# Kernel tuning notes

Measured on AMD Instinct MI355X. Metric: run time of the kernel, lower is better.

## Reference

```python
import jax, jax.numpy as jnp
import numpy as np

N = 50000
E = 800000
F_IN = 128
HID = 64
HEADS = 4
NEG_SLOPE = 0.2  # PyG GATConv default negative_slope


def segment_softmax(e, dst, num_segments):
    # numerically stable softmax over edges grouped by destination node
    m = jax.ops.segment_max(e, dst, num_segments=num_segments)
    ex = jnp.exp(e - m[dst])
    s = jax.ops.segment_sum(ex, dst, num_segments=num_segments)
    return ex / (s[dst] + 1e-16)


def gat_conv(x, src, dst, W, a_src, a_dst, bias, heads, out_ch, concat):
    n = x.shape[0]
    h = (x @ W).reshape(n, heads, out_ch)          # [N,H,C]
    alpha_s = (h * a_src).sum(-1)                  # [N,H]
    alpha_d = (h * a_dst).sum(-1)                  # [N,H]
    e = jax.nn.leaky_relu(alpha_s[src] + alpha_d[dst], NEG_SLOPE)  # [E,H]
    alpha = segment_softmax(e, dst, n)             # [E,H]
    out = jax.ops.segment_sum(h[src] * alpha[:, :, None], dst, num_segments=n)  # [N,H,C]
    out = out.reshape(n, heads * out_ch) if concat else out.mean(axis=1)
    return out + bias


def setup_inputs() -> dict:
    key = jax.random.key(0)
    ks = jax.random.split(key, 16)

    def lin(k, i, o):
        return (jax.random.normal(k, (i, o), jnp.float32) / np.float32(np.sqrt(i)))

    def att(k, h, c):
        return jax.random.normal(k, (h, c), jnp.float32) * np.float32(0.1)

    x = jax.random.normal(ks[0], (N, F_IN), jnp.float32)
    edge_index = jax.random.randint(ks[1], (2, E), 0, N, dtype=jnp.int32)
    return {
        "x": x,
        "W_emb": lin(ks[2], F_IN, HID), "b_emb": jnp.zeros(HID, jnp.float32),
        "W0": lin(ks[3], HID, HEADS * HID), "as0": att(ks[4], HEADS, HID), "ad0": att(ks[5], HEADS, HID), "b0": jnp.zeros(HEADS * HID, jnp.float32),
        "W1": lin(ks[6], HEADS * HID, HEADS * HID), "as1": att(ks[7], HEADS, HID), "ad1": att(ks[8], HEADS, HID), "b1": jnp.zeros(HEADS * HID, jnp.float32),
        "W2": lin(ks[9], HEADS * HID, HID), "as2": att(ks[10], 1, HID), "ad2": att(ks[11], 1, HID), "b2": jnp.zeros(HID, jnp.float32),
        "Wo1": lin(ks[12], HID, HID // 2), "bo1": jnp.zeros(HID // 2, jnp.float32),
        "Wo2": lin(ks[13], HID // 2, 1), "bo2": jnp.zeros(1, jnp.float32),
        "edge_index": edge_index,
    }


def reference(x, W_emb, b_emb, W0, as0, ad0, b0, W1, as1, ad1, b1, W2, as2, ad2, b2, Wo1, bo1, Wo2, bo2, edge_index):
    n = x.shape[0]
    loop = jnp.arange(n, dtype=edge_index.dtype)  # PyG GATConv adds self-loops
    src = jnp.concatenate([edge_index[0], loop])
    dst = jnp.concatenate([edge_index[1], loop])
    h = jax.nn.relu(x @ W_emb + b_emb)
    h = jax.nn.relu(gat_conv(h, src, dst, W0, as0, ad0, b0, HEADS, HID, True))   # dropout=identity (eval)
    h = jax.nn.relu(gat_conv(h, src, dst, W1, as1, ad1, b1, HEADS, HID, True))
    h = gat_conv(h, src, dst, W2, as2, ad2, b2, 1, HID, False)
    h = jax.nn.relu(h @ Wo1 + bo1)
    return h @ Wo2 + bo2  # [N,1]
```

## Files before the change

kernel.cpp:

```cpp
#include <hip/hip_runtime.h>

typedef _Float16 h8_t __attribute__((ext_vector_type(8)));
typedef _Float16 h4_t __attribute__((ext_vector_type(4)));
typedef float floatx4 __attribute__((ext_vector_type(4)));

__device__ __forceinline__ float leaky(float v) { return v >= 0.f ? v : 0.2f * v; }

__global__ void hist_kernel(const int* __restrict__ dst, int E, int* __restrict__ cnt) {
    int e = blockIdx.x * blockDim.x + threadIdx.x;
    if (e < E) atomicAdd(&cnt[dst[e]], 1);
}

__global__ __launch_bounds__(256) void blocksum_kernel(const int* __restrict__ cnt, int N,
                                                       int* __restrict__ bsum) {
    __shared__ int red[256];
    int tid = threadIdx.x;
    int idx = blockIdx.x * 256 + tid;
    red[tid] = idx < N ? cnt[idx] + 1 : 0;
    __syncthreads();
#pragma unroll
    for (int off = 128; off >= 1; off >>= 1) {
        if (tid < off) red[tid] += red[tid + off];
        __syncthreads();
    }
    if (tid == 0) bsum[blockIdx.x] = red[0];
}

__global__ __launch_bounds__(256) void scanbsum_kernel(int* __restrict__ bsum, int nb,
                                                       int* __restrict__ total) {
    __shared__ int part[256];
    int tid = threadIdx.x;
    int per = (nb + 255) / 256;
    int s0 = tid * per, s1 = min(s0 + per, nb);
    int s = 0;
    for (int i = s0; i < s1; i++) s += bsum[i];
    part[tid] = s;
    __syncthreads();
    for (int off = 1; off < 256; off <<= 1) {
        int v = (tid >= off) ? part[tid - off] : 0;
        __syncthreads();
        part[tid] += v;
        __syncthreads();
    }
    int base = (tid == 0) ? 0 : part[tid - 1];
    for (int i = s0; i < s1; i++) {
        int v = bsum[i];
        bsum[i] = base;
        base += v;
    }
    if (tid == 255) *total = part[255];
}

__global__ __launch_bounds__(256) void rowptr_kernel(const int* __restrict__ cnt,
                                                     const int* __restrict__ bsum, int N,
                                                     int* __restrict__ row_ptr,
                                                     int* __restrict__ cursor) {
    __shared__ int lds[256];
    int tid = threadIdx.x;
    int idx = blockIdx.x * 256 + tid;
    int v = idx < N ? cnt[idx] + 1 : 0;
    lds[tid] = v;
    __syncthreads();
    for (int off = 1; off < 256; off <<= 1) {
        int t = (tid >= off) ? lds[tid - off] : 0;
        __syncthreads();
        lds[tid] += t;
        __syncthreads();
    }
    if (idx < N) {
        int p = bsum[blockIdx.x] + lds[tid] - v;
        row_ptr[idx] = p;
        cursor[idx] = p;
    }
}

__global__ void scatter_kernel(const int* __restrict__ src, const int* __restrict__ dst,
                               int E, int N, int* __restrict__ cursor, int* __restrict__ csr_src) {
    int e = blockIdx.x * blockDim.x + threadIdx.x;
    if (e >= E + N) return;
    int s, d;
    if (e < E) { s = src[e]; d = dst[e]; }
    else       { s = e - E;  d = s; }
    int pos = atomicAdd(&cursor[d], 1);
    csr_src[pos] = s;
}

__global__ void prep_weights_all(const float* __restrict__ W_emb, const float* __restrict__ W0,
                                 const float* __restrict__ W1, const float* __restrict__ W2,
                                 _Float16* __restrict__ WeH, _Float16* __restrict__ WeL,
                                 _Float16* __restrict__ W0H, _Float16* __restrict__ W0L,
                                 _Float16* __restrict__ W1H, _Float16* __restrict__ W1L,
                                 _Float16* __restrict__ W2H, _Float16* __restrict__ W2L) {
    int which = blockIdx.y;
    const float* W;
    _Float16 *Wh, *Wl;
    int K, N;
    if (which == 0)      { W = W_emb; Wh = WeH; Wl = WeL; K = 128; N = 64; }
    else if (which == 1) { W = W0;    Wh = W0H; Wl = W0L; K = 64;  N = 256; }
    else if (which == 2) { W = W1;    Wh = W1H; Wl = W1L; K = 256; N = 256; }
    else                 { W = W2;    Wh = W2H; Wl = W2L; K = 256; N = 64; }
    int idx = blockIdx.x * blockDim.x + threadIdx.x;
    if (idx >= K * N) return;
    int k = idx / N, n = idx % N;
    float v = W[idx];
    _Float16 hi = (_Float16)v;
    _Float16 lo = (_Float16)(v - (float)hi);
    size_t o = ((size_t)(k >> 3) * N + n) * 8 + (k & 7);
    Wh[o] = hi; Wl[o] = lo;
}

__global__ void prep_act_kernel(const float* __restrict__ X,
                                _Float16* __restrict__ Ph, _Float16* __restrict__ Pl,
                                int M, int Mpad, int Kg, int K) {
    int idx = blockIdx.x * blockDim.x + threadIdx.x;
    if (idx >= Mpad * Kg) return;
    int row = idx / Kg, kg = idx - row * Kg;
    float vs[8] = {0.f, 0.f, 0.f, 0.f, 0.f, 0.f, 0.f, 0.f};
    if (row < M) {
        const float4* p = (const float4*)(X + (size_t)row * K + kg * 8);
        float4 a = p[0], b = p[1];
        vs[0] = a.x; vs[1] = a.y; vs[2] = a.z; vs[3] = a.w;
        vs[4] = b.x; vs[5] = b.y; vs[6] = b.z; vs[7] = b.w;
    }
    h8_t hh, hl;
#pragma unroll
    for (int j = 0; j < 8; j++) {
        _Float16 hi = (_Float16)vs[j];
        hh[j] = hi;
        hl[j] = (_Float16)(vs[j] - (float)hi);
    }
    size_t o = ((size_t)kg * Mpad + row) * 8;
    *reinterpret_cast<h8_t*>(Ph + o) = hh;
    *reinterpret_cast<h8_t*>(Pl + o) = hl;
}

__global__ __launch_bounds__(256) void gemm_emb_kernel(
        const _Float16* __restrict__ Ah, const _Float16* __restrict__ Al,
        const _Float16* __restrict__ Bh, const _Float16* __restrict__ Bl,
        const float* __restrict__ bias,
        _Float16* __restrict__ Ph, _Float16* __restrict__ Pl,
        int Mpad, int M, int K) {
    const int Nn = 64;
    __shared__ _Float16 Bs[2][4][64][8];
    __shared__ _Float16 stH[4][16][72];
    __shared__ _Float16 stL[4][16][72];
    int tid = threadIdx.x;
    int wv = tid >> 6, lane = tid & 63;
    int m16 = lane & 15, quad = lane >> 4;
    int row0 = blockIdx.x * 128 + wv * 32;

    floatx4 acc[2][4];
#pragma unroll
    for (int t = 0; t < 2; t++)
#pragma unroll
        for (int c = 0; c < 4; c++)
#pragma unroll
            for (int i = 0; i < 4; i++) acc[t][c][i] = 0.f;

    size_t aoff = ((size_t)quad * Mpad + row0 + m16) * 8;
    size_t kqbase = 0;
    const size_t aStep = (size_t)Mpad * 32;
    const size_t bStep = (size_t)Nn * 32;

    for (int kt = 0; kt < K; kt += 32) {
        h8_t ah0 = *reinterpret_cast<const h8_t*>(Ah + aoff);
        h8_t ah1 = *reinterpret_cast<const h8_t*>(Ah + aoff + 128);
        h8_t al0 = *reinterpret_cast<const h8_t*>(Al + aoff);
        h8_t al1 = *reinterpret_cast<const h8_t*>(Al + aoff + 128);
#pragma unroll
        for (int cc = 0; cc < 2; cc++) {
            int c = tid + cc * 256;
            int plane = c >> 8, rem = c & 255, q = rem >> 6, col = rem & 63;
            const _Float16* srcp = (plane ? Bl : Bh) + kqbase + ((size_t)q * Nn + col) * 8;
            *reinterpret_cast<h8_t*>(&Bs[plane][q][col][0]) = *reinterpret_cast<const h8_t*>(srcp);
        }
        __syncthreads();
#pragma unroll
        for (int c = 0; c < 4; c++) {
            h8_t bh = *reinterpret_cast<const h8_t*>(&Bs[0][quad][c * 16 + m16][0]);
            h8_t bl = *reinterpret_cast<const h8_t*>(&Bs[1][quad][c * 16 + m16][0]);
            acc[0][c] = __builtin_amdgcn_mfma_f32_16x16x32_f16(ah0, bh, acc[0][c], 0, 0, 0);
            acc[1][c] = __builtin_amdgcn_mfma_f32_16x16x32_f16(ah1, bh, acc[1][c], 0, 0, 0);
            acc[0][c] = __builtin_amdgcn_mfma_f32_16x16x32_f16(ah0, bl, acc[0][c], 0, 0, 0);
            acc[1][c] = __builtin_amdgcn_mfma_f32_16x16x32_f16(ah1, bl, acc[1][c], 0, 0, 0);
            acc[0][c] = __builtin_amdgcn_mfma_f32_16x16x32_f16(al0, bh, acc[0][c], 0, 0, 0);
            acc[1][c] = __builtin_amdgcn_mfma_f32_16x16x32_f16(al1, bh, acc[1][c], 0, 0, 0);
        }
        __syncthreads();
        aoff += aStep; kqbase += bStep;
    }

#pragma unroll
    for (int t = 0; t < 2; t++) {
#pragma unroll
        for (int c = 0; c < 4; c++) {
            float bv = bias[c * 16 + m16];
#pragma unroll
            for (int i = 0; i < 4; i++) {
                float v = fmaxf(acc[t][c][i] + bv, 0.f);
                _Float16 hi = (_Float16)v;
                stH[wv][quad * 4 + i][c * 16 + m16] = hi;
                stL[wv][quad * 4 + i][c * 16 + m16] = (_Float16)(v - (float)hi);
            }
        }
        __syncthreads();
        int rowChunk = row0 + t * 16;
#pragma unroll
        for (int it = 0; it < 2; it++) {
            int lid = it * 64 + lane;
            int kg = lid >> 4, rloc = lid & 15;
            h8_t vh = *reinterpret_cast<const h8_t*>(&stH[wv][rloc][kg * 8]);
            h8_t vl = *reinterpret_cast<const h8_t*>(&stL[wv][rloc][kg * 8]);
            size_t o = ((size_t)kg * Mpad + rowChunk + rloc) * 8;
            *reinterpret_cast<h8_t*>(Ph + o) = vh;
            *reinterpret_cast<h8_t*>(Pl + o) = vl;
        }
        __syncthreads();
    }
}

template <int TAG>
__global__ __launch_bounds__(256) void gemm_gat_kernel(
        const _Float16* __restrict__ Ah, const _Float16* __restrict__ Al,
        const _Float16* __restrict__ Bh, const _Float16* __restrict__ Bl,
        const float* __restrict__ a_src, const float* __restrict__ a_dst,
        _Float16* __restrict__ hOut, float* __restrict__ aS, float* __restrict__ aD,
        int Mpad, int M, int K) {
    const int Nn = 256;
    __shared__ _Float16 Bs[2][4][128][8];
    __shared__ _Float16 st[4][16][136];
    int tid = threadIdx.x;
    int wv = tid >> 6, lane = tid & 63;
    int m16 = lane & 15, quad = lane >> 4;
    int row0 = blockIdx.x * 128 + wv * 32;
    int colBase = blockIdx.y * 128;

    floatx4 acc[2][8];
#pragma unroll
    for (int t = 0; t < 2; t++)
#pragma unroll
        for (int c = 0; c < 8; c++)
#pragma unroll
            for (int i = 0; i < 4; i++) acc[t][c][i] = 0.f;

    size_t aoff = ((size_t)quad * Mpad + row0 + m16) * 8;
    size_t kqbase = (size_t)colBase * 8;
    const size_t aStep = (size_t)Mpad * 32;
    const size_t bStep = (size_t)Nn * 32;

    for (int kt = 0; kt < K; kt += 32) {
        h8_t ah0 = *reinterpret_cast<const h8_t*>(Ah + aoff);
        h8_t ah1 = *reinterpret_cast<const h8_t*>(Ah + aoff + 128);
        h8_t al0 = *reinterpret_cast<const h8_t*>(Al + aoff);
        h8_t al1 = *reinterpret_cast<const h8_t*>(Al + aoff + 128);
#pragma unroll
        for (int cc = 0; cc < 4; cc++) {
            int c = tid + cc * 256;
            int plane = c >> 9, rem = c & 511, q = rem >> 7, col = rem & 127;
            const _Float16* srcp = (plane ? Bl : Bh) + kqbase + ((size_t)q * Nn + col) * 8;
            *reinterpret_cast<h8_t*>(&Bs[plane][q][col][0]) = *reinterpret_cast<const h8_t*>(srcp);
        }
        __syncthreads();
#pragma unroll
        for (int c = 0; c < 8; c++) {
            h8_t bh = *reinterpret_cast<const h8_t*>(&Bs[0][quad][c * 16 + m16][0]);
            h8_t bl = *reinterpret_cast<const h8_t*>(&Bs[1][quad][c * 16 + m16][0]);
            acc[0][c] = __builtin_amdgcn_mfma_f32_16x16x32_f16(ah0, bh, acc[0][c], 0, 0, 0);
            acc[1][c] = __builtin_amdgcn_mfma_f32_16x16x32_f16(ah1, bh, acc[1][c], 0, 0, 0);
            acc[0][c] = __builtin_amdgcn_mfma_f32_16x16x32_f16(ah0, bl, acc[0][c], 0, 0, 0);
            acc[1][c] = __builtin_amdgcn_mfma_f32_16x16x32_f16(ah1, bl, acc[1][c], 0, 0, 0);
            acc[0][c] = __builtin_amdgcn_mfma_f32_16x16x32_f16(al0, bh, acc[0][c], 0, 0, 0);
            acc[1][c] = __builtin_amdgcn_mfma_f32_16x16x32_f16(al1, bh, acc[1][c], 0, 0, 0);
        }
        __syncthreads();
        aoff += aStep; kqbase += bStep;
    }

    float asv[8], adv[8];
#pragma unroll
    for (int c = 0; c < 8; c++) {
        asv[c] = a_src[colBase + c * 16 + m16];
        adv[c] = a_dst[colBase + c * 16 + m16];
    }
    int hb = colBase >> 6;
#pragma unroll
    for (int t = 0; t < 2; t++) {
#pragma unroll
        for (int i = 0; i < 4; i++) {
            int r = row0 + t * 16 + quad * 4 + i;
            float s0 = 0.f, d0 = 0.f, s1 = 0.f, d1 = 0.f;
#pragma unroll
            for (int c = 0; c < 8; c++) {
                float v = acc[t][c][i];
                if (c < 4) { s0 += v * asv[c]; d0 += v * adv[c]; }
                else       { s1 += v * asv[c]; d1 += v * adv[c]; }
            }
#pragma unroll
            for (int off = 1; off < 16; off <<= 1) {
                s0 += __shfl_xor(s0, off);
                d0 += __shfl_xor(d0, off);
                s1 += __shfl_xor(s1, off);
                d1 += __shfl_xor(d1, off);
            }
            if (m16 == 0 && r < M) {
                aS[r * 4 + hb] = s0;     aD[r * 4 + hb] = d0;
                aS[r * 4 + hb + 1] = s1; aD[r * 4 + hb + 1] = d1;
            }
        }
    }

#pragma unroll
    for (int t = 0; t < 2; t++) {
#pragma unroll
        for (int c = 0; c < 8; c++)
#pragma unroll
            for (int i = 0; i < 4; i++)
                st[wv][quad * 4 + i][c * 16 + m16] = (_Float16)acc[t][c][i];
        __syncthreads();
        int rowChunk = row0 + t * 16;
#pragma unroll
        for (int it = 0; it < 4; it++) {
            int lid = it * 64 + lane;
            int rloc = lid >> 4, u = lid & 15;
            h8_t v = *reinterpret_cast<const h8_t*>(&st[wv][rloc][u * 8]);
            *reinterpret_cast<h8_t*>(hOut + (size_t)(rowChunk + rloc) * 256 + colBase + u * 8) = v;
        }
        __syncthreads();
    }
}

__global__ __launch_bounds__(256) void gemm_l2_kernel(
        const _Float16* __restrict__ Ah, const _Float16* __restrict__ Al,
        const _Float16* __restrict__ Bh, const _Float16* __restrict__ Bl,
        const float* __restrict__ a_src, const float* __restrict__ a_dst,
        _Float16* __restrict__ hOut, float* __restrict__ aS, float* __restrict__ aD,
        int Mpad, int M, int K) {
    const int Nn = 64;
    __shared__ _Float16 Bs[2][4][64][8];
    __shared__ _Float16 st[4][16][72];
    int tid = threadIdx.x;
    int wv = tid >> 6, lane = tid & 63;
    int m16 = lane & 15, quad = lane >> 4;
    int row0 = blockIdx.x * 128 + wv * 32;

    floatx4 acc[2][4];
#pragma unroll
    for (int t = 0; t < 2; t++)
#pragma unroll
        for (int c = 0; c < 4; c++)
#pragma unroll
            for (int i = 0; i < 4; i++) acc[t][c][i] = 0.f;

    size_t aoff = ((size_t)quad * Mpad + row0 + m16) * 8;
    size_t kqbase = 0;
    const size_t aStep = (size_t)Mpad * 32;
    const size_t bStep = (size_t)Nn * 32;

    for (int kt = 0; kt < K; kt += 32) {
        h8_t ah0 = *reinterpret_cast<const h8_t*>(Ah + aoff);
        h8_t ah1 = *reinterpret_cast<const h8_t*>(Ah + aoff + 128);
        h8_t al0 = *reinterpret_cast<const h8_t*>(Al + aoff);
        h8_t al1 = *reinterpret_cast<const h8_t*>(Al + aoff + 128);
#pragma unroll
        for (int cc = 0; cc < 2; cc++) {
            int c = tid + cc * 256;
            int plane = c >> 8, rem = c & 255, q = rem >> 6, col = rem & 63;
            const _Float16* srcp = (plane ? Bl : Bh) + kqbase + ((size_t)q * Nn + col) * 8;
            *reinterpret_cast<h8_t*>(&Bs[plane][q][col][0]) = *reinterpret_cast<const h8_t*>(srcp);
        }
        __syncthreads();
#pragma unroll
        for (int c = 0; c < 4; c++) {
            h8_t bh = *reinterpret_cast<const h8_t*>(&Bs[0][quad][c * 16 + m16][0]);
            h8_t bl = *reinterpret_cast<const h8_t*>(&Bs[1][quad][c * 16 + m16][0]);
            acc[0][c] = __builtin_amdgcn_mfma_f32_16x16x32_f16(ah0, bh, acc[0][c], 0, 0, 0);
            acc[1][c] = __builtin_amdgcn_mfma_f32_16x16x32_f16(ah1, bh, acc[1][c], 0, 0, 0);
            acc[0][c] = __builtin_amdgcn_mfma_f32_16x16x32_f16(ah0, bl, acc[0][c], 0, 0, 0);
            acc[1][c] = __builtin_amdgcn_mfma_f32_16x16x32_f16(ah1, bl, acc[1][c], 0, 0, 0);
            acc[0][c] = __builtin_amdgcn_mfma_f32_16x16x32_f16(al0, bh, acc[0][c], 0, 0, 0);
            acc[1][c] = __builtin_amdgcn_mfma_f32_16x16x32_f16(al1, bh, acc[1][c], 0, 0, 0);
        }
        __syncthreads();
        aoff += aStep; kqbase += bStep;
    }

    float asv[4], adv[4];
#pragma unroll
    for (int c = 0; c < 4; c++) {
        asv[c] = a_src[c * 16 + m16];
        adv[c] = a_dst[c * 16 + m16];
    }
#pragma unroll
    for (int t = 0; t < 2; t++) {
#pragma unroll
        for (int i = 0; i < 4; i++) {
            int r = row0 + t * 16 + quad * 4 + i;
            float s0 = 0.f, d0 = 0.f;
#pragma unroll
            for (int c = 0; c < 4; c++) {
                float v = acc[t][c][i];
                s0 += v * asv[c]; d0 += v * adv[c];
            }
#pragma unroll
            for (int off = 1; off < 16; off <<= 1) {
                s0 += __shfl_xor(s0, off);
                d0 += __shfl_xor(d0, off);
            }
            if (m16 == 0 && r < M) { aS[r] = s0; aD[r] = d0; }
        }
    }

#pragma unroll
    for (int t = 0; t < 2; t++) {
#pragma unroll
        for (int c = 0; c < 4; c++)
#pragma unroll
            for (int i = 0; i < 4; i++)
                st[wv][quad * 4 + i][c * 16 + m16] = (_Float16)acc[t][c][i];
        __syncthreads();
        int rowChunk = row0 + t * 16;
#pragma unroll
        for (int it = 0; it < 2; it++) {
            int lid = it * 64 + lane;
            int rloc = lid >> 3, u = lid & 7;
            h8_t v = *reinterpret_cast<const h8_t*>(&st[wv][rloc][u * 8]);
            *reinterpret_cast<h8_t*>(hOut + (size_t)(rowChunk + rloc) * 64 + u * 8) = v;
        }
        __syncthreads();
    }
}

template <int TAG>
__global__ __launch_bounds__(256) void aggregate4_kernel(const _Float16* __restrict__ hsrc,
                                                         const float* __restrict__ alpha_s,
                                                         const float* __restrict__ alpha_d,
                                                         const int* __restrict__ row_ptr,
                                                         const int* __restrict__ csr_src,
                                                         const float* __restrict__ bias,
                                                         _Float16* __restrict__ outH,
                                                         _Float16* __restrict__ outL,
                                                         int N, int Mpad) {
    __shared__ float wlds[4][64][4];
    __shared__ int   slds[4][64];
    int wv = threadIdx.x >> 6, lane = threadIdx.x & 63;
    int node = blockIdx.x * 4 + wv;
    if (node >= N) return;
    int rs = row_ptr[node], re = row_ptr[node + 1];
    int slot = lane >> 5, lp = lane & 31;
    int ghead = lp >> 3;
    int gbyte = lp * 16;
    float4 ad4 = *(const float4*)(alpha_d + (size_t)node * 4);

    float den0 = 0.f, den1 = 0.f, den2 = 0.f, den3 = 0.f;
    float acc8[8] = {0.f, 0.f, 0.f, 0.f, 0.f, 0.f, 0.f, 0.f};
    float* wp = &wlds[wv][0][0];
    int*   sp = &slds[wv][0];
    const char* hbase = (const char*)hsrc;
    for (int base = rs; base < re; base += 64) {
        int i = base + lane;
        float w0 = 0.f, w1 = 0.f, w2 = 0.f, w3 = 0.f;
        int off = 0;
        if (i < re) {
            int s = csr_src[i];
            float4 as = *(const float4*)(alpha_s + (size_t)s * 4);
            w0 = __expf(fminf(leaky(as.x + ad4.x), 60.f));
            w1 = __expf(fminf(leaky(as.y + ad4.y), 60.f));
            w2 = __expf(fminf(leaky(as.z + ad4.z), 60.f));
            w3 = __expf(fminf(leaky(as.w + ad4.w), 60.f));
            off = s * 512;
        }
        den0 += w0; den1 += w1; den2 += w2; den3 += w3;
        sp[lane] = off;
        *(float4*)(wp + lane * 4) = make_float4(w0, w1, w2, w3);
        int cnt = min(64, re - base);
#pragma unroll 2
        for (int j = slot; j < cnt; j += 2) {
            int o2 = sp[j];
            float w = wp[j * 4 + ghead];
            h8_t hv = *reinterpret_cast<const h8_t*>(hbase + o2 + gbyte);
#pragma unroll
            for (int k = 0; k < 8; k++) acc8[k] += w * (float)hv[k];
        }
    }
#pragma unroll
    for (int k = 0; k < 8; k++) acc8[k] += __shfl_xor(acc8[k], 32);
#pragma unroll
    for (int off = 32; off >= 1; off >>= 1) {
        den0 += __shfl_xor(den0, off);
        den1 += __shfl_xor(den1, off);
        den2 += __shfl_xor(den2, off);
        den3 += __shfl_xor(den3, off);
    }
    if (slot == 0) {
        float den = (ghead & 2) ? ((ghead & 1) ? den3 : den2) : ((ghead & 1) ? den1 : den0);
        float inv = 1.f / (den + 1e-16f);
        int cbase = lp * 8;
        float4 b0 = *(const float4*)(bias + cbase);
        float4 b1 = *(const float4*)(bias + cbase + 4);
        float bv[8] = {b0.x, b0.y, b0.z, b0.w, b1.x, b1.y, b1.z, b1.w};
        h8_t hv, lv;
#pragma unroll
        for (int k = 0; k < 8; k++) {
            float v = fmaxf(acc8[k] * inv + bv[k], 0.f);
            _Float16 hi = (_Float16)v;
            hv[k] = hi;
            lv[k] = (_Float16)(v - (float)hi);
        }
        size_t o = ((size_t)lp * Mpad + node) * 8;
        *reinterpret_cast<h8_t*>(outH + o) = hv;
        *reinterpret_cast<h8_t*>(outL + o) = lv;
    }
}

__global__ __launch_bounds__(256) void aggregate1_kernel(const _Float16* __restrict__ hsrc,
                                                         const float* __restrict__ alpha_s,
                                                         const float* __restrict__ alpha_d,
                                                         const int* __restrict__ row_ptr,
                                                         const int* __restrict__ csr_src,
                                                         const float* __restrict__ bias,
                                                         float* __restrict__ out, int N) {
    __shared__ float wlds[4][64];
    __shared__ int   slds[4][64];
    int wv = threadIdx.x >> 6, lane = threadIdx.x & 63;
    int node = blockIdx.x * 4 + wv;
    if (node >= N) return;
    int rs = row_ptr[node], re = row_ptr[node + 1];
    float ad = alpha_d[node];
    int slot = lane >> 3, lp = lane & 7;
    int gbyte = lp * 16;

    float den = 0.f;
    float acc8[8] = {0.f, 0.f, 0.f, 0.f, 0.f, 0.f, 0.f, 0.f};
    const char* hbase = (const char*)hsrc;
    float* wp = &wlds[wv][0];
    int*   sp = &slds[wv][0];
    for (int base = rs; base < re; base += 64) {
        int i = base + lane;
        float w = 0.f;
        int off = 0;
        if (i < re) {
            int s = csr_src[i];
            w = __expf(fminf(leaky(alpha_s[s] + ad), 60.f));
            off = s * 128;
        }
        den += w;
        sp[lane] = off;
        wp[lane] = w;
        int cnt = min(64, re - base);
#pragma unroll 2
        for (int j = slot; j < cnt; j += 8) {
            float wj = wp[j];
            h8_t hv = *reinterpret_cast<const h8_t*>(hbase + sp[j] + gbyte);
#pragma unroll
            for (int k = 0; k < 8; k++) acc8[k] += wj * (float)hv[k];
        }
    }
#pragma unroll
    for (int k = 0; k < 8; k++) {
        acc8[k] += __shfl_xor(acc8[k], 8);
        acc8[k] += __shfl_xor(acc8[k], 16);
        acc8[k] += __shfl_xor(acc8[k], 32);
    }
#pragma unroll
    for (int off = 32; off >= 1; off >>= 1) den += __shfl_xor(den, off);
    if (slot == 0) {
        float inv = 1.f / (den + 1e-16f);
        int cbase = lp * 8;
        float4 b0 = *(const float4*)(bias + cbase);
        float4 b1 = *(const float4*)(bias + cbase + 4);
        float bv[8] = {b0.x, b0.y, b0.z, b0.w, b1.x, b1.y, b1.z, b1.w};
        float4 o0, o1;
        o0.x = acc8[0] * inv + bv[0]; o0.y = acc8[1] * inv + bv[1];
        o0.z = acc8[2] * inv + bv[2]; o0.w = acc8[3] * inv + bv[3];
        o1.x = acc8[4] * inv + bv[4]; o1.y = acc8[5] * inv + bv[5];
        o1.z = acc8[6] * inv + bv[6]; o1.w = acc8[7] * inv + bv[7];
        float* po = out + (size_t)node * 64 + cbase;
        *(float4*)po = o0;
        *(float4*)(po + 4) = o1;
    }
}

__global__ __launch_bounds__(256) void mlp_head_kernel(const float* __restrict__ hin,
                                                       const float* __restrict__ Wo1,
                                                       const float* __restrict__ bo1,
                                                       const float* __restrict__ Wo2,
                                                       const float* __restrict__ bo2,
                                                       float* __restrict__ out, int N) {
    __shared__ float w1[64 * 32];
    __shared__ float w2[32];
    __shared__ float b1s[32];
    int tid = threadIdx.x;
#pragma unroll
    for (int i = 0; i < 8; i++) w1[tid + i * 256] = Wo1[tid + i * 256];
    if (tid < 32) { w2[tid] = Wo2[tid]; b1s[tid] = bo1[tid]; }
    __syncthreads();
    int n = blockIdx.x * blockDim.x + tid;
    if (n >= N) return;
    float hrow[64];
    const float* pr = hin + (size_t)n * 64;
#pragma unroll
    for (int i = 0; i < 64; i++) hrow[i] = pr[i];
    float sum = 0.f;
    for (int j = 0; j < 32; j++) {
        float a = b1s[j];
#pragma unroll
        for (int k = 0; k < 64; k++) a += hrow[k] * w1[k * 32 + j];
        a = fmaxf(a, 0.f);
        sum += a * w2[j];
    }
    out[n] = sum + bo2[0];
}

extern "C" void kernel_launch(void* const* d_in, const int* in_sizes, int n_in,
                              void* d_out, int out_size, void* d_ws, size_t ws_size,
                              hipStream_t stream) {
    const float* x     = (const float*)d_in[0];
    const float* W_emb = (const float*)d_in[1];
    const float* b_emb = (const float*)d_in[2];
    const float* W0    = (const float*)d_in[3];
    const float* as0   = (const float*)d_in[4];
    const float* ad0   = (const float*)d_in[5];
    const float* b0    = (const float*)d_in[6];
    const float* W1    = (const float*)d_in[7];
    const float* as1   = (const float*)d_in[8];
    const float* ad1   = (const float*)d_in[9];
    const float* b1    = (const float*)d_in[10];
    const float* W2    = (const float*)d_in[11];
    const float* as2   = (const float*)d_in[12];
    const float* ad2   = (const float*)d_in[13];
    const float* b2    = (const float*)d_in[14];
    const float* Wo1   = (const float*)d_in[15];
    const float* bo1   = (const float*)d_in[16];
    const float* Wo2   = (const float*)d_in[17];
    const float* bo2   = (const float*)d_in[18];
    const int* eidx    = (const int*)d_in[19];

    const int N = in_sizes[0] / 128;
    const int E = in_sizes[19] / 2;
    const int* esrc = eidx;
    const int* edst = eidx + E;
    const int gmB  = (N + 127) / 128;
    const int Mpad = gmB * 128;
    const int nb   = (N + 255) / 256;

    char* w = (char*)d_ws;
    auto alloc = [&](size_t bytes) {
        char* p = w;
        w += (bytes + 255) & ~(size_t)255;
        return (void*)p;
    };
    _Float16* hOut = (_Float16*)alloc((size_t)Mpad * 256 * 2);
    _Float16* PHh  = (_Float16*)alloc((size_t)Mpad * 256 * 2);
    _Float16* PHl  = (_Float16*)alloc((size_t)Mpad * 256 * 2);
    _Float16* XPh  = (_Float16*)alloc((size_t)Mpad * 128 * 2);
    _Float16* XPl  = (_Float16*)alloc((size_t)Mpad * 128 * 2);
    float* bufA    = (float*)alloc((size_t)Mpad * 64 * 4);
    float* aS      = (float*)alloc((size_t)N * 4 * 4);
    float* aD      = (float*)alloc((size_t)N * 4 * 4);
    int*   row_ptr = (int*)alloc((size_t)(N + 1) * 4);
    int*   cursor  = (int*)alloc((size_t)N * 4);
    int*   cnt     = (int*)alloc((size_t)N * 4);
    int*   bsum    = (int*)alloc((size_t)nb * 4);
    int*   csr     = (int*)alloc((size_t)(E + N) * 4);
    _Float16* WeH  = (_Float16*)alloc(128 * 64 * 2);
    _Float16* WeL  = (_Float16*)alloc(128 * 64 * 2);
    _Float16* W0H  = (_Float16*)alloc(64 * 256 * 2);
    _Float16* W0L  = (_Float16*)alloc(64 * 256 * 2);
    _Float16* W1H  = (_Float16*)alloc(256 * 256 * 2);
    _Float16* W1L  = (_Float16*)alloc(256 * 256 * 2);
    _Float16* W2H  = (_Float16*)alloc(256 * 64 * 2);
    _Float16* W2L  = (_Float16*)alloc(256 * 64 * 2);

    hipMemsetAsync(cnt, 0, (size_t)N * 4, stream);
    hist_kernel<<<(E + 255) / 256, 256, 0, stream>>>(edst, E, cnt);
    blocksum_kernel<<<nb, 256, 0, stream>>>(cnt, N, bsum);
    scanbsum_kernel<<<1, 256, 0, stream>>>(bsum, nb, row_ptr + N);
    rowptr_kernel<<<nb, 256, 0, stream>>>(cnt, bsum, N, row_ptr, cursor);
    scatter_kernel<<<(E + N + 255) / 256, 256, 0, stream>>>(esrc, edst, E, N, cursor, csr);

    prep_weights_all<<<dim3(256, 4), 256, 0, stream>>>(W_emb, W0, W1, W2,
                                                       WeH, WeL, W0H, W0L, W1H, W1L, W2H, W2L);

    int gn4 = (N + 3) / 4;

    prep_act_kernel<<<((size_t)Mpad * 16 + 255) / 256, 256, 0, stream>>>(x, XPh, XPl, N, Mpad, 16, 128);
    gemm_emb_kernel<<<dim3(gmB, 1), 256, 0, stream>>>(XPh, XPl, WeH, WeL, b_emb, PHh, PHl, Mpad, N, 128);

    gemm_gat_kernel<0><<<dim3(gmB, 2), 256, 0, stream>>>(PHh, PHl, W0H, W0L, as0, ad0, hOut, aS, aD, Mpad, N, 64);
    aggregate4_kernel<0><<<gn4, 256, 0, stream>>>(hOut, aS, aD, row_ptr, csr, b0, PHh, PHl, N, Mpad);

    gemm_gat_kernel<1><<<dim3(gmB, 2), 256, 0, stream>>>(PHh, PHl, W1H, W1L, as1, ad1, hOut, aS, aD, Mpad, N, 256);
    aggregate4_kernel<1><<<gn4, 256, 0, stream>>>(hOut, aS, aD, row_ptr, csr, b1, PHh, PHl, N, Mpad);

    gemm_l2_kernel<<<dim3(gmB, 1), 256, 0, stream>>>(PHh, PHl, W2H, W2L, as2, ad2, hOut, aS, aD, Mpad, N, 256);
    aggregate1_kernel<<<gn4, 256, 0, stream>>>(hOut, aS, aD, row_ptr, csr, b2, bufA, N);

    mlp_head_kernel<<<(N + 255) / 256, 256, 0, stream>>>(bufA, Wo1, bo1, Wo2, bo2, (float*)d_out, N);
}
```

Baseline: 488.5 us.

## Fuse activation split into embedding GEMM and merge final aggregation with MLP head

Result: no change. 484.5 us (-0.8%).

```diff
diff --git a/kernel.cpp b/kernel.cpp
--- a/kernel.cpp
+++ b/kernel.cpp
@@ -109,39 +109,14 @@
     Wh[o] = hi; Wl[o] = lo;
 }
 
-__global__ void prep_act_kernel(const float* __restrict__ X,
-                                _Float16* __restrict__ Ph, _Float16* __restrict__ Pl,
-                                int M, int Mpad, int Kg, int K) {
-    int idx = blockIdx.x * blockDim.x + threadIdx.x;
-    if (idx >= Mpad * Kg) return;
-    int row = idx / Kg, kg = idx - row * Kg;
-    float vs[8] = {0.f, 0.f, 0.f, 0.f, 0.f, 0.f, 0.f, 0.f};
-    if (row < M) {
-        const float4* p = (const float4*)(X + (size_t)row * K + kg * 8);
-        float4 a = p[0], b = p[1];
-        vs[0] = a.x; vs[1] = a.y; vs[2] = a.z; vs[3] = a.w;
-        vs[4] = b.x; vs[5] = b.y; vs[6] = b.z; vs[7] = b.w;
-    }
-    h8_t hh, hl;
-#pragma unroll
-    for (int j = 0; j < 8; j++) {
-        _Float16 hi = (_Float16)vs[j];
-        hh[j] = hi;
-        hl[j] = (_Float16)(vs[j] - (float)hi);
-    }
-    size_t o = ((size_t)kg * Mpad + row) * 8;
-    *reinterpret_cast<h8_t*>(Ph + o) = hh;
-    *reinterpret_cast<h8_t*>(Pl + o) = hl;
-}
-
 __global__ __launch_bounds__(256) void gemm_emb_kernel(
-        const _Float16* __restrict__ Ah, const _Float16* __restrict__ Al,
+        const float* __restrict__ X,
         const _Float16* __restrict__ Bh, const _Float16* __restrict__ Bl,
         const float* __restrict__ bias,
         _Float16* __restrict__ Ph, _Float16* __restrict__ Pl,
-        int Mpad, int M, int K) {
-    const int Nn = 64;
-    __shared__ _Float16 Bs[2][4][64][8];
+        int Mpad, int M) {
+    const int Nn = 64, K = 128;
+    __shared__ _Float16 Bs[2][16][64][8];
     __shared__ _Float16 stH[4][16][72];
     __shared__ _Float16 stL[4][16][72];
     int tid = threadIdx.x;
@@ -149,6 +124,15 @@
     int m16 = lane & 15, quad = lane >> 4;
     int row0 = blockIdx.x * 128 + wv * 32;
 
+#pragma unroll
+    for (int cc = 0; cc < 8; cc++) {
+        int c = tid + cc * 256;
+        int plane = c >> 10, rem = c & 1023, q = rem >> 6, col = rem & 63;
+        const _Float16* srcp = (plane ? Bl : Bh) + ((size_t)q * Nn + col) * 8;
+        *reinterpret_cast<h8_t*>(&Bs[plane][q][col][0]) = *reinterpret_cast<const h8_t*>(srcp);
+    }
+    __syncthreads();
+
     floatx4 acc[2][4];
 #pragma unroll
     for (int t = 0; t < 2; t++)
@@ -157,28 +141,36 @@
 #pragma unroll
             for (int i = 0; i < 4; i++) acc[t][c][i] = 0.f;
 
-    size_t aoff = ((size_t)quad * Mpad + row0 + m16) * 8;
-    size_t kqbase = 0;
-    const size_t aStep = (size_t)Mpad * 32;
-    const size_t bStep = (size_t)Nn * 32;
-
-    for (int kt = 0; kt < K; kt += 32) {
-        h8_t ah0 = *reinterpret_cast<const h8_t*>(Ah + aoff);
-        h8_t ah1 = *reinterpret_cast<const h8_t*>(Ah + aoff + 128);
-        h8_t al0 = *reinterpret_cast<const h8_t*>(Al + aoff);
-        h8_t al1 = *reinterpret_cast<const h8_t*>(Al + aoff + 128);
-#pragma unroll
-        for (int cc = 0; cc < 2; cc++) {
-            int c = tid + cc * 256;
-            int plane = c >> 8, rem = c & 255, q = rem >> 6, col = rem & 63;
-            const _Float16* srcp = (plane ? Bl : Bh) + kqbase + ((size_t)q * Nn + col) * 8;
-            *reinterpret_cast<h8_t*>(&Bs[plane][q][col][0]) = *reinterpret_cast<const h8_t*>(srcp);
-        }
-        __syncthreads();
+    int r0 = row0 + m16, r1 = row0 + 16 + m16;
+#pragma unroll
+    for (int kt4 = 0; kt4 < 4; kt4++) {
+        int kcol = kt4 * 32 + quad * 8;
+        float vs0[8] = {0,0,0,0,0,0,0,0}, vs1[8] = {0,0,0,0,0,0,0,0};
+        if (r0 < M) {
+            const float4* p = (const float4*)(X + (size_t)r0 * K + kcol);
+            float4 a = p[0], b = p[1];
+            vs0[0]=a.x; vs0[1]=a.y; vs0[2]=a.z; vs0[3]=a.w;
+            vs0[4]=b.x; vs0[5]=b.y; vs0[6]=b.z; vs0[7]=b.w;
+        }
+        if (r1 < M) {
+            const float4* p = (const float4*)(X + (size_t)r1 * K + kcol);
+            float4 a = p[0], b = p[1];
+            vs1[0]=a.x; vs1[1]=a.y; vs1[2]=a.z; vs1[3]=a.w;
+            vs1[4]=b.x; vs1[5]=b.y; vs1[6]=b.z; vs1[7]=b.w;
+        }
+        h8_t ah0, al0, ah1, al1;
+#pragma unroll
+        for (int j = 0; j < 8; j++) {
+            _Float16 hi0 = (_Float16)vs0[j];
+            ah0[j] = hi0; al0[j] = (_Float16)(vs0[j] - (float)hi0);
+            _Float16 hi1 = (_Float16)vs1[j];
+            ah1[j] = hi1; al1[j] = (_Float16)(vs1[j] - (float)hi1);
+        }
+        int kq = kt4 * 4 + quad;
 #pragma unroll
         for (int c = 0; c < 4; c++) {
-            h8_t bh = *reinterpret_cast<const h8_t*>(&Bs[0][quad][c * 16 + m16][0]);
-            h8_t bl = *reinterpret_cast<const h8_t*>(&Bs[1][quad][c * 16 + m16][0]);
+            h8_t bh = *reinterpret_cast<const h8_t*>(&Bs[0][kq][c * 16 + m16][0]);
+            h8_t bl = *reinterpret_cast<const h8_t*>(&Bs[1][kq][c * 16 + m16][0]);
             acc[0][c] = __builtin_amdgcn_mfma_f32_16x16x32_f16(ah0, bh, acc[0][c], 0, 0, 0);
             acc[1][c] = __builtin_amdgcn_mfma_f32_16x16x32_f16(ah1, bh, acc[1][c], 0, 0, 0);
             acc[0][c] = __builtin_amdgcn_mfma_f32_16x16x32_f16(ah0, bl, acc[0][c], 0, 0, 0);
@@ -186,8 +178,6 @@
             acc[0][c] = __builtin_amdgcn_mfma_f32_16x16x32_f16(al0, bh, acc[0][c], 0, 0, 0);
             acc[1][c] = __builtin_amdgcn_mfma_f32_16x16x32_f16(al1, bh, acc[1][c], 0, 0, 0);
         }
-        __syncthreads();
-        aoff += aStep; kqbase += bStep;
     }
 
 #pragma unroll
@@ -219,8 +209,114 @@
     }
 }
 
-template <int TAG>
-__global__ __launch_bounds__(256) void gemm_gat_kernel(
+__global__ __launch_bounds__(256) void gemm_gat0_kernel(
+        const _Float16* __restrict__ Ah, const _Float16* __restrict__ Al,
+        const _Float16* __restrict__ Bh, const _Float16* __restrict__ Bl,
+        const float* __restrict__ a_src, const float* __restrict__ a_dst,
+        _Float16* __restrict__ hOut, float* __restrict__ aS, float* __restrict__ aD,
+        int Mpad, int M) {
+    const int Nn = 256;
+    __shared__ _Float16 Bs[2][8][128][8];
+    __shared__ _Float16 st[4][16][136];
+    int tid = threadIdx.x;
+    int wv = tid >> 6, lane = tid & 63;
+    int m16 = lane & 15, quad = lane >> 4;
+    int row0 = blockIdx.x * 128 + wv * 32;
+    int colBase = blockIdx.y * 128;
+    size_t kqbase = (size_t)colBase * 8;
+
+#pragma unroll
+    for (int cc = 0; cc < 8; cc++) {
+        int c = tid + cc * 256;
+        int plane = c >> 10, rem = c & 1023, q = rem >> 7, col = rem & 127;
+        const _Float16* srcp = (plane ? Bl : Bh) + kqbase + ((size_t)q * Nn + col) * 8;
+        *reinterpret_cast<h8_t*>(&Bs[plane][q][col][0]) = *reinterpret_cast<const h8_t*>(srcp);
+    }
+    __syncthreads();
+
+    floatx4 acc[2][8];
+#pragma unroll
+    for (int t = 0; t < 2; t++)
+#pragma unroll
+        for (int c = 0; c < 8; c++)
+#pragma unroll
+            for (int i = 0; i < 4; i++) acc[t][c][i] = 0.f;
+
+#pragma unroll
+    for (int kt = 0; kt < 2; kt++) {
+        int kq = kt * 4 + quad;
+        size_t aoff = ((size_t)kq * Mpad + row0 + m16) * 8;
+        h8_t ah0 = *reinterpret_cast<const h8_t*>(Ah + aoff);
+        h8_t ah1 = *reinterpret_cast<const h8_t*>(Ah + aoff + 128);
+        h8_t al0 = *reinterpret_cast<const h8_t*>(Al + aoff);
+        h8_t al1 = *reinterpret_cast<const h8_t*>(Al + aoff + 128);
+#pragma unroll
+        for (int c = 0; c < 8; c++) {
+            h8_t bh = *reinterpret_cast<const h8_t*>(&Bs[0][kq][c * 16 + m16][0]);
+            h8_t bl = *reinterpret_cast<const h8_t*>(&Bs[1][kq][c * 16 + m16][0]);
+            acc[0][c] = __builtin_amdgcn_mfma_f32_16x16x32_f16(ah0, bh, acc[0][c], 0, 0, 0);
+            acc[1][c] = __builtin_amdgcn_mfma_f32_16x16x32_f16(ah1, bh, acc[1][c], 0, 0, 0);
+            acc[0][c] = __builtin_amdgcn_mfma_f32_16x16x32_f16(ah0, bl, acc[0][c], 0, 0, 0);
+            acc[1][c] = __builtin_amdgcn_mfma_f32_16x16x32_f16(ah1, bl, acc[1][c], 0, 0, 0);
+            acc[0][c] = __builtin_amdgcn_mfma_f32_16x16x32_f16(al0, bh, acc[0][c], 0, 0, 0);
+            acc[1][c] = __builtin_amdgcn_mfma_f32_16x16x32_f16(al1, bh, acc[1][c], 0, 0, 0);
+        }
+    }
+
+    float asv[8], adv[8];
+#pragma unroll
+    for (int c = 0; c < 8; c++) {
+        asv[c] = a_src[colBase + c * 16 + m16];
+        adv[c] = a_dst[colBase + c * 16 + m16];
+    }
+    int hb = colBase >> 6;
+#pragma unroll
+    for (int t = 0; t < 2; t++) {
+#pragma unroll
+        for (int i = 0; i < 4; i++) {
+            int r = row0 + t * 16 + quad * 4 + i;
+            float s0 = 0.f, d0 = 0.f, s1 = 0.f, d1 = 0.f;
+#pragma unroll
+            for (int c = 0; c < 8; c++) {
+                float v = acc[t][c][i];
+                if (c < 4) { s0 += v * asv[c]; d0 += v * adv[c]; }
+                else       { s1 += v * asv[c]; d1 += v * adv[c]; }
+            }
+#pragma unroll
+            for (int off = 1; off < 16; off <<= 1) {
+                s0 += __shfl_xor(s0, off);
+                d0 += __shfl_xor(d0, off);
+                s1 += __shfl_xor(s1, off);
+                d1 += __shfl_xor(d1, off);
+            }
+            if (m16 == 0 && r < M) {
+                aS[r * 4 + hb] = s0;     aD[r * 4 + hb] = d0;
+                aS[r * 4 + hb + 1] = s1; aD[r * 4 + hb + 1] = d1;
+            }
+        }
+    }
+
+#pragma unroll
+    for (int t = 0; t < 2; t++) {
+#pragma unroll
+        for (int c = 0; c < 8; c++)
+#pragma unroll
+            for (int i = 0; i < 4; i++)
+                st[wv][quad * 4 + i][c * 16 + m16] = (_Float16)acc[t][c][i];
+        __syncthreads();
+        int rowChunk = row0 + t * 16;
+#pragma unroll
+        for (int it = 0; it < 4; it++) {
+            int lid = it * 64 + lane;
+            int rloc = lid >> 4, u = lid & 15;
+            h8_t v = *reinterpret_cast<const h8_t*>(&st[wv][rloc][u * 8]);
+            *reinterpret_cast<h8_t*>(hOut + (size_t)(rowChunk + rloc) * 256 + colBase + u * 8) = v;
+        }
+        __syncthreads();
+    }
+}
+
+__global__ __launch_bounds__(256) void gemm_gat1_kernel(
         const _Float16* __restrict__ Ah, const _Float16* __restrict__ Al,
         const _Float16* __restrict__ Bh, const _Float16* __restrict__ Bl,
         const float* __restrict__ a_src, const float* __restrict__ a_dst,
@@ -512,16 +608,30 @@
     }
 }
 
-__global__ __launch_bounds__(256) void aggregate1_kernel(const _Float16* __restrict__ hsrc,
-                                                         const float* __restrict__ alpha_s,
-                                                         const float* __restrict__ alpha_d,
-                                                         const int* __restrict__ row_ptr,
-                                                         const int* __restrict__ csr_src,
-                                                         const float* __restrict__ bias,
-                                                         float* __restrict__ out, int N) {
+__global__ __launch_bounds__(256) void agg1_mlp_kernel(const _Float16* __restrict__ hsrc,
+                                                       const float* __restrict__ alpha_s,
+                                                       const float* __restrict__ alpha_d,
+                                                       const int* __restrict__ row_ptr,
+                                                       const int* __restrict__ csr_src,
+                                                       const float* __restrict__ bias,
+                                                       const float* __restrict__ Wo1,
+                                                       const float* __restrict__ bo1,
+                                                       const float* __restrict__ Wo2,
+                                                       const float* __restrict__ bo2,
+                                                       float* __restrict__ out, int N) {
     __shared__ float wlds[4][64];
     __shared__ int   slds[4][64];
-    int wv = threadIdx.x >> 6, lane = threadIdx.x & 63;
+    __shared__ float hrow[4][64];
+    __shared__ float w1s[64 * 32];
+    __shared__ float w2s[32];
+    __shared__ float b1s[32];
+    int tid = threadIdx.x;
+#pragma unroll
+    for (int i = 0; i < 8; i++) w1s[tid + i * 256] = Wo1[tid + i * 256];
+    if (tid < 32) { w2s[tid] = Wo2[tid]; b1s[tid] = bo1[tid]; }
+    __syncthreads();
+
+    int wv = tid >> 6, lane = tid & 63;
     int node = blockIdx.x * 4 + wv;
     if (node >= N) return;
     int rs = row_ptr[node], re = row_ptr[node + 1];
@@ -566,49 +676,19 @@
     if (slot == 0) {
         float inv = 1.f / (den + 1e-16f);
         int cbase = lp * 8;
-        float4 b0 = *(const float4*)(bias + cbase);
-        float4 b1 = *(const float4*)(bias + cbase + 4);
-        float bv[8] = {b0.x, b0.y, b0.z, b0.w, b1.x, b1.y, b1.z, b1.w};
-        float4 o0, o1;
-        o0.x = acc8[0] * inv + bv[0]; o0.y = acc8[1] * inv + bv[1];
-        o0.z = acc8[2] * inv + bv[2]; o0.w = acc8[3] * inv + bv[3];
-        o1.x = acc8[4] * inv + bv[4]; o1.y = acc8[5] * inv + bv[5];
-        o1.z = acc8[6] * inv + bv[6]; o1.w = acc8[7] * inv + bv[7];
-        float* po = out + (size_t)node * 64 + cbase;
-        *(float4*)po = o0;
-        *(float4*)(po + 4) = o1;
-    }
-}
-
-__global__ __launch_bounds__(256) void mlp_head_kernel(const float* __restrict__ hin,
-                                                       const float* __restrict__ Wo1,
-                                                       const float* __restrict__ bo1,
-                                                       const float* __restrict__ Wo2,
-                                                       const float* __restrict__ bo2,
-                                                       float* __restrict__ out, int N) {
-    __shared__ float w1[64 * 32];
-    __shared__ float w2[32];
-    __shared__ float b1s[32];
-    int tid = threadIdx.x;
-#pragma unroll
-    for (int i = 0; i < 8; i++) w1[tid + i * 256] = Wo1[tid + i * 256];
-    if (tid < 32) { w2[tid] = Wo2[tid]; b1s[tid] = bo1[tid]; }
-    __syncthreads();
-    int n = blockIdx.x * blockDim.x + tid;
-    if (n >= N) return;
-    float hrow[64];
-    const float* pr = hin + (size_t)n * 64;
-#pragma unroll
-    for (int i = 0; i < 64; i++) hrow[i] = pr[i];
-    float sum = 0.f;
-    for (int j = 0; j < 32; j++) {
-        float a = b1s[j];
-#pragma unroll
-        for (int k = 0; k < 64; k++) a += hrow[k] * w1[k * 32 + j];
-        a = fmaxf(a, 0.f);
-        sum += a * w2[j];
-    }
-    out[n] = sum + bo2[0];
+#pragma unroll
+        for (int k = 0; k < 8; k++)
+            hrow[wv][cbase + k] = acc8[k] * inv + bias[cbase + k];
+    }
+    int j = lane & 31;
+    float a = b1s[j];
+#pragma unroll 4
+    for (int k = 0; k < 64; k++) a += hrow[wv][k] * w1s[k * 32 + j];
+    a = fmaxf(a, 0.f);
+    float p = a * w2s[j];
+#pragma unroll
+    for (int off = 16; off >= 1; off >>= 1) p += __shfl_xor(p, off);
+    if (lane == 0) out[node] = p + bo2[0];
 }
 
 extern "C" void kernel_launch(void* const* d_in, const int* in_sizes, int n_in,
@@ -652,9 +732,6 @@
     _Float16* hOut = (_Float16*)alloc((size_t)Mpad * 256 * 2);
     _Float16* PHh  = (_Float16*)alloc((size_t)Mpad * 256 * 2);
     _Float16* PHl  = (_Float16*)alloc((size_t)Mpad * 256 * 2);
-    _Float16* XPh  = (_Float16*)alloc((size_t)Mpad * 128 * 2);
-    _Float16* XPl  = (_Float16*)alloc((size_t)Mpad * 128 * 2);
-    float* bufA    = (float*)alloc((size_t)Mpad * 64 * 4);
     float* aS      = (float*)alloc((size_t)N * 4 * 4);
     float* aD      = (float*)alloc((size_t)N * 4 * 4);
     int*   row_ptr = (int*)alloc((size_t)(N + 1) * 4);
@@ -683,17 +760,15 @@
 
     int gn4 = (N + 3) / 4;
 
-    prep_act_kernel<<<((size_t)Mpad * 16 + 255) / 256, 256, 0, stream>>>(x, XPh, XPl, N, Mpad, 16, 128);
-    gemm_emb_kernel<<<dim3(gmB, 1), 256, 0, stream>>>(XPh, XPl, WeH, WeL, b_emb, PHh, PHl, Mpad, N, 128);
-
-    gemm_gat_kernel<0><<<dim3(gmB, 2), 256, 0, stream>>>(PHh, PHl, W0H, W0L, as0, ad0, hOut, aS, aD, Mpad, N, 64);
+    gemm_emb_kernel<<<dim3(gmB, 1), 256, 0, stream>>>(x, WeH, WeL, b_emb, PHh, PHl, Mpad, N);
+
+    gemm_gat0_kernel<<<dim3(gmB, 2), 256, 0, stream>>>(PHh, PHl, W0H, W0L, as0, ad0, hOut, aS, aD, Mpad, N);
     aggregate4_kernel<0><<<gn4, 256, 0, stream>>>(hOut, aS, aD, row_ptr, csr, b0, PHh, PHl, N, Mpad);
 
-    gemm_gat_kernel<1><<<dim3(gmB, 2), 256, 0, stream>>>(PHh, PHl, W1H, W1L, as1, ad1, hOut, aS, aD, Mpad, N, 256);
+    gemm_gat1_kernel<<<dim3(gmB, 2), 256, 0, stream>>>(PHh, PHl, W1H, W1L, as1, ad1, hOut, aS, aD, Mpad, N, 256);
     aggregate4_kernel<1><<<gn4, 256, 0, stream>>>(hOut, aS, aD, row_ptr, csr, b1, PHh, PHl, N, Mpad);
 
     gemm_l2_kernel<<<dim3(gmB, 1), 256, 0, stream>>>(PHh, PHl, W2H, W2L, as2, ad2, hOut, aS, aD, Mpad, N, 256);
-    aggregate1_kernel<<<gn4, 256, 0, stream>>>(hOut, aS, aD, row_ptr, csr, b2, bufA, N);
-
-    mlp_head_kernel<<<(N + 255) / 256, 256, 0, stream>>>(bufA, Wo1, bo1, Wo2, bo2, (float*)d_out, N);
-}
+    agg1_mlp_kernel<<<gn4, 256, 0, stream>>>(hOut, aS, aD, row_ptr, csr, b2,
+                                             Wo1, bo1, Wo2, bo2, (float*)d_out, N);
+}
```
